# Performance work log

Measured on AMD Instinct MI355X. Metric: run time of the kernel, lower is better.

Reference implementation:

```python
import math
import jax, jax.numpy as jnp
import numpy as np

N_EMBD = 1024
N_HEAD = 16
EPS = 1e-5


def get_alibi_slopes(n_head):
    def pow2_slopes(n):
        start = 2 ** (-2 ** (-(math.log2(n) - 3)))
        return [start * start ** i for i in range(n)]
    if math.log2(n_head).is_integer():
        slopes = pow2_slopes(n_head)
    else:
        c = 2 ** math.floor(math.log2(n_head))
        slopes = pow2_slopes(c)
        extra = pow2_slopes(2 * c)[0::2]
        slopes.extend(extra[: n_head - c])
    return jnp.asarray(slopes, dtype=jnp.float32)


def layernorm(x, w, b):
    mu = jnp.mean(x, axis=-1, keepdims=True)
    var = jnp.var(x, axis=-1, keepdims=True)
    return (x - mu) * jax.lax.rsqrt(var + EPS) * w + b


def setup_inputs() -> dict:
    key = jax.random.key(0)
    ks = jax.random.split(key, 8)
    C = N_EMBD
    B, T = 2, 2048
    s = 0.02
    return {
        "x": jax.random.normal(ks[0], (B, T, C), dtype=jnp.float32),
        "ln1_w": jnp.ones((C,), jnp.float32),
        "ln1_b": jnp.zeros((C,), jnp.float32),
        "w_qkv": jax.random.normal(ks[1], (C, 3 * C), dtype=jnp.float32) * s,
        "b_qkv": jnp.zeros((3 * C,), jnp.float32),
        "w_proj": jax.random.normal(ks[2], (C, C), dtype=jnp.float32) * s,
        "b_proj": jnp.zeros((C,), jnp.float32),
        "ln2_w": jnp.ones((C,), jnp.float32),
        "ln2_b": jnp.zeros((C,), jnp.float32),
        "w_fc": jax.random.normal(ks[3], (C, 4 * C), dtype=jnp.float32) * s,
        "b_fc": jnp.zeros((4 * C,), jnp.float32),
        "w_fc2": jax.random.normal(ks[4], (4 * C, C), dtype=jnp.float32) * s,
        "b_fc2": jnp.zeros((C,), jnp.float32),
    }


def reference(x, ln1_w, ln1_b, w_qkv, b_qkv, w_proj, b_proj,
              ln2_w, ln2_b, w_fc, b_fc, w_fc2, b_fc2):
    B, T, C = x.shape
    H = N_HEAD
    D = C // H

    # --- attention with ALiBi ---
    h = layernorm(x, ln1_w, ln1_b)
    qkv = h @ w_qkv + b_qkv                       # [B,T,3C]
    q, k, v = jnp.split(qkv, 3, axis=-1)
    q = q.reshape(B, T, H, D).transpose(0, 2, 1, 3)  # [B,H,T,D]
    k = k.reshape(B, T, H, D).transpose(0, 2, 1, 3)
    v = v.reshape(B, T, H, D).transpose(0, 2, 1, 3)

    att = jnp.einsum('bhqd,bhkd->bhqk', q, k) * (1.0 / math.sqrt(D))

    pos = jnp.arange(T, dtype=jnp.float32)
    distances = pos[:, None] - pos[None, :]        # [T,T], i-j
    slopes = get_alibi_slopes(H)[:, None, None]     # [H,1,1]
    bias = slopes * distances[None, :, :]           # [H,T,T]
    causal = jnp.triu(jnp.ones((T, T), dtype=bool), k=1)
    bias = jnp.where(causal[None, :, :], -jnp.inf, bias)

    att = jax.nn.softmax(att + bias[None], axis=-1)
    y = jnp.einsum('bhqk,bhkd->bhqd', att, v)
    y = y.transpose(0, 2, 1, 3).reshape(B, T, C)
    x = x + y @ w_proj + b_proj

    # --- MLP ---
    h = layernorm(x, ln2_w, ln2_b)
    h = jax.nn.gelu(h @ w_fc + b_fc, approximate=False)
    x = x + h @ w_fc2 + b_fc2
    return x
```

## Files before the change

kernel.cpp:

```cpp
#include <hip/hip_runtime.h>
#include <hip/hip_bf16.h>
#include <math.h>

#define N_EMBD 1024
#define N_HEADC 16
#define HEAD_D 64

typedef __attribute__((ext_vector_type(8))) short short8;
typedef __attribute__((ext_vector_type(4))) float floatx4;

__device__ __forceinline__ ushort f2b(float f) {
    __hip_bfloat16 h = __float2bfloat16(f);
    return *reinterpret_cast<ushort*>(&h);
}

__device__ __forceinline__ void async_cp16(const void* gsrc, void* ldst) {
    __builtin_amdgcn_global_load_lds(
        (const __attribute__((address_space(1))) void*)gsrc,
        (__attribute__((address_space(3))) void*)ldst, 16, 0, 0);
}

__device__ __forceinline__ int xcd_swizzle(int bid, int nwg) {
    const int q = nwg >> 3, r = nwg & 7;
    const int xcd = bid & 7, loc = bid >> 3;
    return (xcd < r ? xcd * (q + 1) : r * (q + 1) + (xcd - r) * q) + loc;
}

template <int CTRL>
__device__ __forceinline__ float dppf(float x) {
    int r = __builtin_amdgcn_update_dpp(0, __builtin_bit_cast(int, x),
                                        CTRL, 0xF, 0xF, true);
    return __builtin_bit_cast(float, r);
}
__device__ __forceinline__ float redmax16(float x) {
    x = fmaxf(x, dppf<0xB1>(x));
    x = fmaxf(x, dppf<0x4E>(x));
    x = fmaxf(x, dppf<0x141>(x));
    x = fmaxf(x, dppf<0x140>(x));
    return x;
}
__device__ __forceinline__ float redsum16(float x) {
    x += dppf<0xB1>(x);
    x += dppf<0x4E>(x);
    x += dppf<0x141>(x);
    x += dppf<0x140>(x);
    return x;
}

__global__ __launch_bounds__(256) void ln_kernel(const float* __restrict__ x,
                                                 const float* __restrict__ w,
                                                 const float* __restrict__ b,
                                                 ushort* __restrict__ out) {
    const int row = blockIdx.x;
    const int t = threadIdx.x;
    const float4 v = reinterpret_cast<const float4*>(x + (size_t)row * N_EMBD)[t];
    float s  = v.x + v.y + v.z + v.w;
    float ss = v.x * v.x + v.y * v.y + v.z * v.z + v.w * v.w;
    for (int o = 32; o > 0; o >>= 1) {
        s  += __shfl_down(s, o);
        ss += __shfl_down(ss, o);
    }
    __shared__ float as_[4], ass_[4];
    const int wid = t >> 6, lane = t & 63;
    if (lane == 0) { as_[wid] = s; ass_[wid] = ss; }
    __syncthreads();
    const float ts  = as_[0] + as_[1] + as_[2] + as_[3];
    const float tss = ass_[0] + ass_[1] + ass_[2] + ass_[3];
    const float mu  = ts * (1.f / N_EMBD);
    const float var = tss * (1.f / N_EMBD) - mu * mu;
    const float inv = rsqrtf(var + 1e-5f);
    const float4 wv = reinterpret_cast<const float4*>(w)[t];
    const float4 bv = reinterpret_cast<const float4*>(b)[t];
    ushort4 o;
    o.x = f2b((v.x - mu) * inv * wv.x + bv.x);
    o.y = f2b((v.y - mu) * inv * wv.y + bv.y);
    o.z = f2b((v.z - mu) * inv * wv.z + bv.z);
    o.w = f2b((v.w - mu) * inv * wv.w + bv.w);
    reinterpret_cast<ushort4*>(out + (size_t)row * N_EMBD)[t] = o;
}

__global__ void convtrans_kernel(const float* __restrict__ W,
                                 ushort* __restrict__ Wt, int K, int N) {
    __shared__ float tile[32][33];
    const int tid = threadIdx.x;
    const int r = tid >> 3;
    const int c4 = (tid & 7) * 4;
    const int bx = blockIdx.x, by = blockIdx.y;

    float4 v = *(const float4*)&W[((size_t)(by * 32 + r)) * N + bx * 32 + c4];
    tile[r][c4 + 0] = v.x; tile[r][c4 + 1] = v.y;
    tile[r][c4 + 2] = v.z; tile[r][c4 + 3] = v.w;
    __syncthreads();

    ushort4 u;
    u.x = f2b(tile[c4 + 0][r]); u.y = f2b(tile[c4 + 1][r]);
    u.z = f2b(tile[c4 + 2][r]); u.w = f2b(tile[c4 + 3][r]);
    *(ushort4*)&Wt[((size_t)(bx * 32 + r)) * K + by * 32 + c4] = u;
}

__device__ __forceinline__ void gemm_stage(
        const ushort* __restrict__ A, const ushort* __restrict__ Bt,
        ushort* As, ushort* Bs,
        int m0, int n0, int K, int k0, int w, int lane) {
#pragma unroll
    for (int l = 0; l < 2; l++) {
        const int cbase = w * 128 + l * 64;
        const int c = cbase + lane;
        const int row = c >> 2, kc8 = (c & 3) * 8;
        async_cp16(A  + (size_t)(m0 + row) * K + k0 + kc8, &As[cbase * 8]);
        async_cp16(Bt + (size_t)(n0 + row) * K + k0 + kc8, &Bs[cbase * 8]);
    }
}

__device__ __forceinline__ void gemm_compute(
        const ushort* As, const ushort* Bs, floatx4 (*acc)[4],
        int wm, int wn, int quad, int l16) {
    short8 a[4], bf[4];
#pragma unroll
    for (int i = 0; i < 4; i++)
        a[i] = *(const short8*)&As[(wm * 64 + i * 16 + l16) * 32 + quad * 8];
#pragma unroll
    for (int j = 0; j < 4; j++)
        bf[j] = *(const short8*)&Bs[(wn * 64 + j * 16 + l16) * 32 + quad * 8];
#pragma unroll
    for (int i = 0; i < 4; i++)
#pragma unroll
        for (int j = 0; j < 4; j++)
            acc[i][j] = __builtin_amdgcn_mfma_f32_16x16x32_bf16(
                a[i], bf[j], acc[i][j], 0, 0, 0);
}

__global__ __launch_bounds__(256) void gemm_bf16_kernel(
        const ushort* __restrict__ A,
        const ushort* __restrict__ Bt,
        const float* __restrict__ bias,
        const float* __restrict__ residual,
        float* __restrict__ out32,
        ushort* __restrict__ out16,
        int M, int N, int K, int do_gelu) {
    __shared__ ushort As[2][128 * 32];
    __shared__ ushort Bs[2][128 * 32];

    const int tid  = threadIdx.x;
    const int w    = tid >> 6;
    const int lane = tid & 63;
    const int quad = lane >> 4;
    const int l16  = lane & 15;
    const int wm   = w >> 1;
    const int wn   = w & 1;

    int bid = blockIdx.y * gridDim.x + blockIdx.x;
    bid = xcd_swizzle(bid, gridDim.x * gridDim.y);
    const int bx = bid % gridDim.x;
    const int by = bid / gridDim.x;
    const int m0 = by * 128;
    const int n0 = bx * 128;

    const int kchunk = K / gridDim.z;
    const int kbeg   = blockIdx.z * kchunk;
    if (gridDim.z > 1)
        out32 += (size_t)blockIdx.z * M * N;

    floatx4 acc[4][4];
#pragma unroll
    for (int i = 0; i < 4; i++)
#pragma unroll
        for (int j = 0; j < 4; j++) acc[i][j] = (floatx4){0.f, 0.f, 0.f, 0.f};

    const int nt = kchunk >> 5;

    gemm_stage(A, Bt, As[0], Bs[0], m0, n0, K, kbeg, w, lane);
    __syncthreads();

    for (int t = 0; t < nt; t += 2) {
        gemm_stage(A, Bt, As[1], Bs[1], m0, n0, K, kbeg + ((t + 1) << 5), w, lane);
        gemm_compute(As[0], Bs[0], acc, wm, wn, quad, l16);
        __syncthreads();
        if (t + 2 < nt)
            gemm_stage(A, Bt, As[0], Bs[0], m0, n0, K, kbeg + ((t + 2) << 5), w, lane);
        gemm_compute(As[1], Bs[1], acc, wm, wn, quad, l16);
        __syncthreads();
    }

#pragma unroll
    for (int i = 0; i < 4; i++) {
#pragma unroll
        for (int j = 0; j < 4; j++) {
            const int nn = n0 + wn * 64 + j * 16 + l16;
            const float bv = bias ? bias[nn] : 0.f;
#pragma unroll
            for (int r = 0; r < 4; r++) {
                const int mm = m0 + wm * 64 + i * 16 + quad * 4 + r;
                float v = acc[i][j][r] + bv;
                if (do_gelu) v = 0.5f * v * (1.f + erff(v * 0.70710678118654752f));
                if (residual) v += residual[(size_t)mm * N + nn];
                if (out32) out32[(size_t)mm * N + nn] = v;
                if (out16) out16[(size_t)mm * N + nn] = f2b(v);
            }
        }
    }
}

__global__ __launch_bounds__(256) void combine_kernel(
        const float* __restrict__ p0, const float* __restrict__ p1,
        const float* __restrict__ bias, float* __restrict__ out) {
    const int i = blockIdx.x * 256 + threadIdx.x;
    const float4 a = ((const float4*)p0)[i];
    const float4 c = ((const float4*)p1)[i];
    const float4 bb = ((const float4*)bias)[i & 255];
    float4 o = ((float4*)out)[i];
    o.x += a.x + c.x + bb.x;
    o.y += a.y + c.y + bb.y;
    o.z += a.z + c.z + bb.z;
    o.w += a.w + c.w + bb.w;
    ((float4*)out)[i] = o;
}

#define AT_PAD 72
#define LOG2E 1.4426950408889634f

__device__ __forceinline__ void attn_tile_step(
        short8 aq0, short8 aq1,
        ushort (*__restrict__ Ks)[AT_PAD],
        ushort (*__restrict__ Vt)[AT_PAD],
        ushort (*__restrict__ Ps)[AT_PAD],
        float* m_r, float* l_r, floatx4* acc,
        int q0, int kt, bool domask,
        float qs2, float slope2, const float* skb,
        int w, int quad, int l16) {
    floatx4 sfrag[4];
#pragma unroll
    for (int kb = 0; kb < 4; kb++) {
        const int kcol = kb * 16 + l16;
        short8 bk0 = *(const short8*)&Ks[kcol][quad * 8];
        short8 bk1 = *(const short8*)&Ks[kcol][32 + quad * 8];
        floatx4 s = (floatx4){0.f, 0.f, 0.f, 0.f};
        s = __builtin_amdgcn_mfma_f32_16x16x32_bf16(aq0, bk0, s, 0, 0, 0);
        s = __builtin_amdgcn_mfma_f32_16x16x32_bf16(aq1, bk1, s, 0, 0, 0);
        sfrag[kb] = s;
    }

    const int psw = ((w * 4 + quad) & 7) << 3;
    int pcol[4];
#pragma unroll
    for (int kb = 0; kb < 4; kb++) pcol[kb] = (kb * 16 + l16) ^ psw;

    const float ktb = (float)(kt * 64);
#pragma unroll
    for (int r = 0; r < 4; r++) {
        const int q = q0 + w * 16 + quad * 4 + r;
        const float rowc = slope2 * ((float)q - ktb);
        float sv[4];
        float rm = -INFINITY;
#pragma unroll
        for (int kb = 0; kb < 4; kb++) {
            float s = fmaf(sfrag[kb][r], qs2, rowc) - skb[kb];
            if (domask) {
                const int k = kt * 64 + kb * 16 + l16;
                s = (k <= q) ? s : -INFINITY;
            }
            sv[kb] = s;
            rm = fmaxf(rm, s);
        }
        rm = redmax16(rm);
        if (rm > m_r[r]) {
            const float corr = exp2f(m_r[r] - rm);
            m_r[r] = rm;
            l_r[r] *= corr;
#pragma unroll
            for (int db = 0; db < 4; db++) acc[db][r] *= corr;
        }
        float rs = 0.f;
#pragma unroll
        for (int kb = 0; kb < 4; kb++) {
            const float pv = exp2f(sv[kb] - m_r[r]);
            rs += pv;
            Ps[w * 16 + quad * 4 + r][pcol[kb]] = f2b(pv);
        }
        rs = redsum16(rs);
        l_r[r] += rs;
    }

    const int prw = ((w * 4 + (l16 >> 2)) & 7) << 3;
    short8 ap0 = *(const short8*)&Ps[w * 16 + l16][(quad * 8) ^ prw];
    short8 ap1 = *(const short8*)&Ps[w * 16 + l16][(32 + quad * 8) ^ prw];
#pragma unroll
    for (int db = 0; db < 4; db++) {
        const int dv = db * 16 + l16;
        const int svw = ((db * 4 + (l16 >> 2)) & 7) << 3;
        short8 bv0 = *(const short8*)&Vt[dv][(quad * 8) ^ svw];
        short8 bv1 = *(const short8*)&Vt[dv][(32 + quad * 8) ^ svw];
        acc[db] = __builtin_amdgcn_mfma_f32_16x16x32_bf16(ap0, bv0, acc[db], 0, 0, 0);
        acc[db] = __builtin_amdgcn_mfma_f32_16x16x32_bf16(ap1, bv1, acc[db], 0, 0, 0);
    }
}

__global__ __launch_bounds__(256) void attn_mfma_kernel(
        const ushort* __restrict__ qkv, ushort* __restrict__ y, int B, int T) {
    const int C3 = 3 * N_EMBD;
    const int NT = T / 64;

    const int gx = gridDim.x, gxy = gridDim.x * gridDim.y;
    int lin = blockIdx.z * gxy + blockIdx.y * gx + blockIdx.x;
    lin = xcd_swizzle(lin, gxy * gridDim.z);
    const int p = lin % gx;
    const int h = (lin / gx) % gridDim.y;
    const int b = lin / gxy;

    const int qt = NT - 1 - p;
    const int tid  = threadIdx.x;
    const int lane = tid & 63;
    const int w    = tid >> 6;
    const int quad = lane >> 4;
    const int l16  = lane & 15;

    __shared__ ushort QPs[64][AT_PAD];
    __shared__ ushort Ks[64][AT_PAD];
    __shared__ ushort Vt[64][AT_PAD];

    const float slope  = exp2f(-0.5f * (float)(h + 1));
    const float slope2 = slope * LOG2E;
    const float qs2    = 0.125f * LOG2E;
    float skb[4];
#pragma unroll
    for (int kb = 0; kb < 4; kb++) skb[kb] = slope2 * (float)(kb * 16 + l16);

    const int q0 = qt * 64;
    const size_t hb = (size_t)b * T * C3 + (size_t)h * HEAD_D;

    int srow[4], sd0[4], svr[4];
#pragma unroll
    for (int i = 0; i < 4; i++) {
        const int idx = tid + i * 256;
        srow[i] = idx >> 4;
        sd0[i]  = (idx & 15) * 4;
        svr[i]  = srow[i] ^ ((idx & 7) << 3);
    }

#pragma unroll
    for (int i = 0; i < 4; i++) {
        *(ushort4*)&QPs[srow[i]][sd0[i]] =
            *(const ushort4*)&qkv[hb + (size_t)(q0 + srow[i]) * C3 + sd0[i]];
    }
    __syncthreads();

    const int mrow = w * 16 + l16;
    short8 aq0 = *(const short8*)&QPs[mrow][quad * 8];
    short8 aq1 = *(const short8*)&QPs[mrow][32 + quad * 8];

    float m_r[4], l_r[4];
    floatx4 acc[4];
#pragma unroll
    for (int r = 0; r < 4; r++) {
        m_r[r] = -INFINITY; l_r[r] = 0.f;
        acc[r] = (floatx4){0.f, 0.f, 0.f, 0.f};
    }

#pragma unroll
    for (int i = 0; i < 4; i++) {
        const size_t src = hb + (size_t)srow[i] * C3 + sd0[i];
        *(ushort4*)&Ks[srow[i]][sd0[i]] = *(const ushort4*)&qkv[src + N_EMBD];
        ushort4 vv = *(const ushort4*)&qkv[src + 2 * N_EMBD];
        Vt[sd0[i] + 0][svr[i]] = vv.x;
        Vt[sd0[i] + 1][svr[i]] = vv.y;
        Vt[sd0[i] + 2][svr[i]] = vv.z;
        Vt[sd0[i] + 3][svr[i]] = vv.w;
    }
    __syncthreads();

    for (int kt = 0; kt <= qt; kt++) {
        ushort4 kreg[4], vreg[4];
        const bool pf = (kt < qt);
        if (pf) {
#pragma unroll
            for (int i = 0; i < 4; i++) {
                const size_t src =
                    hb + (size_t)((kt + 1) * 64 + srow[i]) * C3 + sd0[i];
                kreg[i] = *(const ushort4*)&qkv[src + N_EMBD];
                vreg[i] = *(const ushort4*)&qkv[src + 2 * N_EMBD];
            }
        }

        attn_tile_step(aq0, aq1, Ks, Vt, QPs, m_r, l_r, acc,
                       q0, kt, kt == qt, qs2, slope2, skb, w, quad, l16);
        __syncthreads();

        if (pf) {
#pragma unroll
            for (int i = 0; i < 4; i++) {
                *(ushort4*)&Ks[srow[i]][sd0[i]] = kreg[i];
                Vt[sd0[i] + 0][svr[i]] = vreg[i].x;
                Vt[sd0[i] + 1][svr[i]] = vreg[i].y;
                Vt[sd0[i] + 2][svr[i]] = vreg[i].z;
                Vt[sd0[i] + 3][svr[i]] = vreg[i].w;
            }
        }
        __syncthreads();
    }

#pragma unroll
    for (int r = 0; r < 4; r++) {
        const int qa = q0 + w * 16 + quad * 4 + r;
        const float ia = 1.f / l_r[r];
#pragma unroll
        for (int db = 0; db < 4; db++) {
            y[((size_t)b * T + qa) * N_EMBD + h * HEAD_D + db * 16 + l16] =
                f2b(acc[db][r] * ia);
        }
    }
}

extern "C" void kernel_launch(void* const* d_in, const int* in_sizes, int n_in,
                              void* d_out, int out_size, void* d_ws, size_t ws_size,
                              hipStream_t stream) {
    const int B = 2, T = 2048, C = N_EMBD;
    const int M = B * T;

    const float* x      = (const float*)d_in[0];
    const float* ln1_w  = (const float*)d_in[1];
    const float* ln1_b  = (const float*)d_in[2];
    const float* w_qkv  = (const float*)d_in[3];
    const float* b_qkv  = (const float*)d_in[4];
    const float* w_proj = (const float*)d_in[5];
    const float* b_proj = (const float*)d_in[6];
    const float* ln2_w  = (const float*)d_in[7];
    const float* ln2_b  = (const float*)d_in[8];
    const float* w_fc   = (const float*)d_in[9];
    const float* b_fc   = (const float*)d_in[10];
    const float* w_fc2  = (const float*)d_in[11];
    const float* b_fc2  = (const float*)d_in[12];
    float* out = (float*)d_out;

    char* ws = (char*)d_ws;
    size_t off = 0;
    ushort* wt_qkv  = (ushort*)(ws + off); off += (size_t)3 * C * C * 2;
    ushort* wt_proj = (ushort*)(ws + off); off += (size_t)C * C * 2;
    ushort* wt_fc   = (ushort*)(ws + off); off += (size_t)4 * C * C * 2;
    ushort* wt_fc2  = (ushort*)(ws + off); off += (size_t)4 * C * C * 2;
    ushort* h16     = (ushort*)(ws + off); off += (size_t)M * C * 2;
    ushort* qkv16   = (ushort*)(ws + off); off += (size_t)M * 3 * C * 2;
    ushort* y16     = (ushort*)(ws + off); off += (size_t)M * C * 2;
    ushort* fc16    = (ushort*)(ws + off); off += (size_t)M * 4 * C * 2;

    convtrans_kernel<<<dim3(3 * C / 32, C / 32), 256, 0, stream>>>(w_qkv, wt_qkv, C, 3 * C);
    convtrans_kernel<<<dim3(C / 32, C / 32), 256, 0, stream>>>(w_proj, wt_proj, C, C);
    convtrans_kernel<<<dim3(4 * C / 32, C / 32), 256, 0, stream>>>(w_fc, wt_fc, C, 4 * C);
    convtrans_kernel<<<dim3(C / 32, 4 * C / 32), 256, 0, stream>>>(w_fc2, wt_fc2, 4 * C, C);

    ln_kernel<<<M, 256, 0, stream>>>(x, ln1_w, ln1_b, h16);

    gemm_bf16_kernel<<<dim3(3 * C / 128, M / 128), 256, 0, stream>>>(
        h16, wt_qkv, b_qkv, nullptr, nullptr, qkv16, M, 3 * C, C, 0);

    attn_mfma_kernel<<<dim3(T / 64, N_HEADC, B), 256, 0, stream>>>(
        qkv16, y16, B, T);

    gemm_bf16_kernel<<<dim3(C / 128, M / 128), 256, 0, stream>>>(
        y16, wt_proj, b_proj, x, out, nullptr, M, C, C, 0);

    ln_kernel<<<M, 256, 0, stream>>>(out, ln2_w, ln2_b, h16);

    gemm_bf16_kernel<<<dim3(4 * C / 128, M / 128), 256, 0, stream>>>(
        h16, wt_fc, b_fc, nullptr, nullptr, fc16, M, 4 * C, C, 1);

    float* part = (float*)h16;
    gemm_bf16_kernel<<<dim3(C / 128, M / 128, 2), 256, 0, stream>>>(
        fc16, wt_fc2, nullptr, nullptr, part, nullptr, M, C, 4 * C, 0);
    combine_kernel<<<(M * C) / (256 * 4), 256, 0, stream>>>(
        part, part + (size_t)M * C, b_fc2, out);
}
```

Measured before the change: 443.7 us.

## Split long causal attention query tiles across two blocks with a combine pass

Query tiles 16-31 now have their key range split in two halves, each handled by its own block that writes an unnormalized partial output plus running max and sum to scratch (reusing the fc16 buffer). A new combine kernel merges the two halves with log-sum-exp weighting and writes bf16 output. The aim is to balance the causal triangle's uneven work and raise block count, so the longest tiles stop dominating the tail. The cost is extra fp32 partial traffic, one more launch, and duplicated Q loads.

```diff
diff --git a/kernel.cpp b/kernel.cpp
--- a/kernel.cpp
+++ b/kernel.cpp
@@ -296,18 +296,32 @@
 }
 
 __global__ __launch_bounds__(256) void attn_mfma_kernel(
-        const ushort* __restrict__ qkv, ushort* __restrict__ y, int B, int T) {
+        const ushort* __restrict__ qkv, ushort* __restrict__ y,
+        float* __restrict__ opart, float* __restrict__ mpart,
+        float* __restrict__ lpart, int B, int T) {
     const int C3 = 3 * N_EMBD;
-    const int NT = T / 64;
-
-    const int gx = gridDim.x, gxy = gridDim.x * gridDim.y;
-    int lin = blockIdx.z * gxy + blockIdx.y * gx + blockIdx.x;
-    lin = xcd_swizzle(lin, gxy * gridDim.z);
-    const int p = lin % gx;
-    const int h = (lin / gx) % gridDim.y;
-    const int b = lin / gxy;
-
-    const int qt = NT - 1 - p;
+
+    const int lin = xcd_swizzle(blockIdx.x, gridDim.x);
+    const int bh = lin / 48;
+    const int s  = lin % 48;
+    int qt, cc, ktb_i, kte;
+    bool split;
+    if (s < 32) {
+        split = true;
+        qt = 31 - (s >> 1);
+        cc = s & 1;
+        const int hc = (qt + 2) >> 1;
+        ktb_i = cc ? hc : 0;
+        kte   = cc ? qt : hc - 1;
+    } else {
+        split = false;
+        qt = 47 - s;
+        cc = 0;
+        ktb_i = 0;
+        kte = qt;
+    }
+    const int b = bh >> 4, h = bh & 15;
+
     const int tid  = threadIdx.x;
     const int lane = tid & 63;
     const int w    = tid >> 6;
@@ -358,7 +372,7 @@
 
 #pragma unroll
     for (int i = 0; i < 4; i++) {
-        const size_t src = hb + (size_t)srow[i] * C3 + sd0[i];
+        const size_t src = hb + (size_t)(ktb_i * 64 + srow[i]) * C3 + sd0[i];
         *(ushort4*)&Ks[srow[i]][sd0[i]] = *(const ushort4*)&qkv[src + N_EMBD];
         ushort4 vv = *(const ushort4*)&qkv[src + 2 * N_EMBD];
         Vt[sd0[i] + 0][svr[i]] = vv.x;
@@ -368,9 +382,9 @@
     }
     __syncthreads();
 
-    for (int kt = 0; kt <= qt; kt++) {
+    for (int kt = ktb_i; kt <= kte; kt++) {
         ushort4 kreg[4], vreg[4];
-        const bool pf = (kt < qt);
+        const bool pf = (kt < kte);
         if (pf) {
 #pragma unroll
             for (int i = 0; i < 4; i++) {
@@ -398,15 +412,64 @@
         __syncthreads();
     }
 
-#pragma unroll
-    for (int r = 0; r < 4; r++) {
-        const int qa = q0 + w * 16 + quad * 4 + r;
-        const float ia = 1.f / l_r[r];
-#pragma unroll
-        for (int db = 0; db < 4; db++) {
-            y[((size_t)b * T + qa) * N_EMBD + h * HEAD_D + db * 16 + l16] =
-                f2b(acc[db][r] * ia);
-        }
+    if (!split) {
+#pragma unroll
+        for (int r = 0; r < 4; r++) {
+            const int qa = q0 + w * 16 + quad * 4 + r;
+            const float ia = 1.f / l_r[r];
+#pragma unroll
+            for (int db = 0; db < 4; db++) {
+                y[((size_t)b * T + qa) * N_EMBD + h * HEAD_D + db * 16 + l16] =
+                    f2b(acc[db][r] * ia);
+            }
+        }
+    } else {
+        const int pidx = (bh * 16 + (qt - 16)) * 2 + cc;
+#pragma unroll
+        for (int r = 0; r < 4; r++) {
+            const int row = w * 16 + quad * 4 + r;
+#pragma unroll
+            for (int db = 0; db < 4; db++) {
+                opart[((size_t)pidx * 64 + row) * 64 + db * 16 + l16] =
+                    acc[db][r];
+            }
+            if (l16 == 0) {
+                mpart[pidx * 64 + row] = m_r[r];
+                lpart[pidx * 64 + row] = l_r[r];
+            }
+        }
+    }
+}
+
+__global__ __launch_bounds__(256) void attn_combine_kernel(
+        const float* __restrict__ opart, const float* __restrict__ mpart,
+        const float* __restrict__ lpart, ushort* __restrict__ y, int T) {
+    const int x  = blockIdx.x;
+    const int bh = x >> 4;
+    const int qt = 16 + (x & 15);
+    const int b  = bh >> 4, h = bh & 15;
+    const int t  = threadIdx.x;
+    const int row = t >> 2;
+    const int dq  = (t & 3) << 4;
+    const int p0 = x * 2, p1 = p0 + 1;
+
+    const float m0 = mpart[p0 * 64 + row], m1 = mpart[p1 * 64 + row];
+    const float l0 = lpart[p0 * 64 + row], l1 = lpart[p1 * 64 + row];
+    const float M  = fmaxf(m0, m1);
+    const float w0 = exp2f(m0 - M), w1 = exp2f(m1 - M);
+    const float inv = 1.f / (l0 * w0 + l1 * w1);
+
+    const float* o0 = &opart[((size_t)p0 * 64 + row) * 64 + dq];
+    const float* o1 = &opart[((size_t)p1 * 64 + row) * 64 + dq];
+    ushort* yr = &y[((size_t)b * T + qt * 64 + row) * N_EMBD + h * HEAD_D + dq];
+#pragma unroll
+    for (int j = 0; j < 16; j += 4) {
+        const float4 a = *(const float4*)&o0[j];
+        const float4 c = *(const float4*)&o1[j];
+        yr[j + 0] = f2b((a.x * w0 + c.x * w1) * inv);
+        yr[j + 1] = f2b((a.y * w0 + c.y * w1) * inv);
+        yr[j + 2] = f2b((a.z * w0 + c.z * w1) * inv);
+        yr[j + 3] = f2b((a.w * w0 + c.w * w1) * inv);
     }
 }
 
@@ -452,8 +515,12 @@
     gemm_bf16_kernel<<<dim3(3 * C / 128, M / 128), 256, 0, stream>>>(
         h16, wt_qkv, b_qkv, nullptr, nullptr, qkv16, M, 3 * C, C, 0);
 
-    attn_mfma_kernel<<<dim3(T / 64, N_HEADC, B), 256, 0, stream>>>(
-        qkv16, y16, B, T);
+    float* aop = (float*)fc16;
+    float* amp = aop + (size_t)1024 * 64 * 64;
+    float* alp = amp + (size_t)1024 * 64;
+    attn_mfma_kernel<<<32 * 48, 256, 0, stream>>>(
+        qkv16, y16, aop, amp, alp, B, T);
+    attn_combine_kernel<<<512, 256, 0, stream>>>(aop, amp, alp, y16, T);
 
     gemm_bf16_kernel<<<dim3(C / 128, M / 128), 256, 0, stream>>>(
         y16, wt_proj, b_proj, x, out, nullptr, M, C, C, 0);
```

Result: no change. 437.0 us (-1.5%).
